# Optimization experiments

Measured on AMD Instinct MI355X. Metric: run time of the kernel, lower is better.

The kernel has to match this reference:

```python
import jax, jax.numpy as jnp
import numpy as np


def setup_inputs() -> dict:
    key = jax.random.key(0)
    k1, k2 = jax.random.split(key)
    B, H, S, D = 2, 16, 2048, 64
    scores = jax.random.normal(k1, (B, H, S, S), dtype=jnp.float32)
    v = jax.random.normal(k2, (B, H, S, D), dtype=jnp.float32)
    return {"scores": scores, "v": v}


def reference(scores, v):
    # softmax over last dim of [B,H,S,S], then contract with V [B,H,S,D]
    prob = jax.nn.softmax(scores, axis=-1)
    return jnp.einsum('bhqk,bhkd->bhqd', prob, v)
```

## Files before the change

kernel.cpp:

```cpp
#include <hip/hip_runtime.h>
#include <hip/hip_bf16.h>

#define NBH     32
#define SEQ     2048
#define DIM     64
#define QBLK    64
#define KBLK    128
#define NCHUNK  (SEQ / KBLK)
#define PSTR    136

typedef __attribute__((ext_vector_type(4))) float f32x4;
typedef __attribute__((ext_vector_type(8))) short bf16x8;

__device__ __forceinline__ unsigned short bfbits(float f) {
    return __builtin_bit_cast(unsigned short, __float2bfloat16(f));
}

__global__ __launch_bounds__(256)
void vprep_kernel(const float* __restrict__ v, unsigned short* __restrict__ wsv)
{
    const int blk = blockIdx.x;
    const int bh  = blk >> 5, tau = blk & 31;
    const float* vp = v + ((size_t)bh * SEQ + tau * 64) * DIM;
    unsigned short* op = wsv + (size_t)blk * 4096;

    for (int fl = threadIdx.x; fl < 512; fl += 256) {
        const int ks1 = fl >> 8, dt = (fl >> 6) & 3, lane = fl & 63;
        const int g = lane >> 4, c = lane & 15;
        const float* sp = vp + (ks1 * 32 + g * 8) * DIM + dt * 16 + c;
        bf16x8 frag;
#pragma unroll
        for (int j = 0; j < 8; ++j)
            frag[j] = (short)bfbits(sp[j * DIM]);
        *reinterpret_cast<bf16x8*>(op + fl * 8) = frag;
    }
}

__global__ __launch_bounds__(256, 2)
void softmaxv_kernel(const float* __restrict__ scores,
                     const unsigned short* __restrict__ vfrags,
                     float* __restrict__ out)
{
    __shared__ unsigned short p_lds[4][2][16 * PSTR];
    __shared__ float l_lds[4][16];

    const int tid  = threadIdx.x;
    const int w    = tid >> 6;
    const int lane = tid & 63;
    const int g    = lane >> 4;
    const int c    = lane & 15;
    const int h    = lane >> 5;
    const int c2   = lane & 31;

    const int bid = blockIdx.x;
    const int nb  = (bid & 7) * (NBH * 32 / 8) + (bid >> 3);
    const int bh  = nb >> 5;
    const int qb  = nb & 31;
    const int q0  = qb * QBLK;

    const float* sp = scores + ((size_t)bh * SEQ + q0 + w * 16 + h) * SEQ + c2 * 4;
    const unsigned short* vb = vfrags + (size_t)bh * 32 * 4096 + lane * 8;

    unsigned short* pb0 = &p_lds[w][0][0];
    unsigned short* pb1 = &p_lds[w][1][0];

    float lsum[8] = {0.f, 0.f, 0.f, 0.f, 0.f, 0.f, 0.f, 0.f};
    f32x4 acc[4];
#pragma unroll
    for (int dt = 0; dt < 4; ++dt) acc[dt] = (f32x4)0.0f;

#define SLOADS(dst, t)                                                         \
    {                                                                          \
        _Pragma("unroll")                                                      \
        for (int j = 0; j < 8; ++j)                                            \
            dst[j] = *reinterpret_cast<const f32x4*>(                          \
                sp + (size_t)(2 * j) * SEQ + (t) * KBLK);                      \
    }

#define VLOAD(vf, t)                                                           \
    {                                                                          \
        _Pragma("unroll")                                                      \
        for (int ks = 0; ks < 4; ++ks)                                         \
            _Pragma("unroll")                                                  \
            for (int dt = 0; dt < 4; ++dt)                                     \
                vf[ks][dt] = *reinterpret_cast<const bf16x8*>(                 \
                    vb + (size_t)(2 * (t) + (ks >> 1)) * 4096 +                \
                    ((ks & 1) * 4 + dt) * 512);                                \
    }

#define PROC(sreg, pbuf)                                                       \
    {                                                                          \
        _Pragma("unroll")                                                      \
        for (int j = 0; j < 8; ++j) {                                          \
            f32x4 s4 = sreg[j];                                                \
            float p0 = __expf(s4[0]);                                          \
            float p1 = __expf(s4[1]);                                          \
            float p2 = __expf(s4[2]);                                          \
            float p3 = __expf(s4[3]);                                          \
            lsum[j] += (p0 + p1) + (p2 + p3);                                  \
            unsigned lo = (unsigned)bfbits(p0) | ((unsigned)bfbits(p1) << 16); \
            unsigned hi = (unsigned)bfbits(p2) | ((unsigned)bfbits(p3) << 16); \
            *reinterpret_cast<uint2*>(&pbuf[(2 * j + h) * PSTR + c2 * 4]) =    \
                make_uint2(lo, hi);                                            \
        }                                                                      \
        _Pragma("unroll")                                                      \
        for (int ks = 0; ks < 4; ++ks) {                                       \
            const bf16x8 a = *reinterpret_cast<const bf16x8*>(                 \
                &pbuf[c * PSTR + ks * 32 + g * 8]);                            \
            _Pragma("unroll")                                                  \
            for (int dt = 0; dt < 4; ++dt)                                     \
                acc[dt] = __builtin_amdgcn_mfma_f32_16x16x32_bf16(             \
                    a, vf[ks][dt], acc[dt], 0, 0, 0);                          \
        }                                                                      \
    }

    f32x4 sA[8], sB[8];
    bf16x8 vf[4][4];
    SLOADS(sA, 0)
    for (int t = 0; t < NCHUNK; t += 2) {
        VLOAD(vf, t)
        SLOADS(sB, t + 1)
        PROC(sA, pb0)
        VLOAD(vf, t + 1)
        if (t + 2 < NCHUNK) SLOADS(sA, t + 2)
        PROC(sB, pb1)
    }
#undef SLOADS
#undef VLOAD
#undef PROC

#pragma unroll
    for (int j = 0; j < 8; ++j) {
        float l = lsum[j];
        l += __shfl_xor(l, 1);
        l += __shfl_xor(l, 2);
        l += __shfl_xor(l, 4);
        l += __shfl_xor(l, 8);
        l += __shfl_xor(l, 16);
        if (c2 == j) l_lds[w][2 * j + h] = l;
    }

    float* op = out + ((size_t)bh * SEQ + q0 + w * 16) * DIM;
    float rl[4];
#pragma unroll
    for (int r = 0; r < 4; ++r)
        rl[r] = 1.0f / l_lds[w][g * 4 + r];
#pragma unroll
    for (int dt = 0; dt < 4; ++dt)
#pragma unroll
        for (int r = 0; r < 4; ++r)
            op[(g * 4 + r) * DIM + dt * 16 + c] = acc[dt][r] * rl[r];
}

extern "C" void kernel_launch(void* const* d_in, const int* in_sizes, int n_in,
                              void* d_out, int out_size, void* d_ws, size_t ws_size,
                              hipStream_t stream)
{
    const float* scores = (const float*)d_in[0];
    const float* v      = (const float*)d_in[1];
    float* out          = (float*)d_out;
    unsigned short* wsv = (unsigned short*)d_ws;

    vprep_kernel<<<dim3(NBH * 32), dim3(256), 0, stream>>>(v, wsv);
    softmaxv_kernel<<<dim3(NBH * (SEQ / QBLK)), dim3(256), 0, stream>>>(scores, wsv, out);
}
```

Before: 137.8 us.

## Compute softmax row sums via MFMA with ones vector and widen key chunks

Each key chunk grows from 128 to 256 columns, so every lane loads full contiguous 16-byte segments across 16 rows. The per-row exp sums are no longer accumulated in scalar registers and reduced with shuffles at the end. An extra MFMA against a vector of bf16 ones accumulates them, and V fragments are streamed in quarter-chunk pieces between MFMA groups. This removes scalar adds and the final cross-lane reduction but adds MFMA work and doubles score register pressure (32 f32x4), which may lower occupancy. The denominator now sums bf16-rounded probabilities rather than fp32 values.

```diff
diff --git a/kernel.cpp b/kernel.cpp
--- a/kernel.cpp
+++ b/kernel.cpp
@@ -5,9 +5,9 @@
 #define SEQ     2048
 #define DIM     64
 #define QBLK    64
-#define KBLK    128
+#define KBLK    256
 #define NCHUNK  (SEQ / KBLK)
-#define PSTR    136
+#define PSTR    264
 
 typedef __attribute__((ext_vector_type(4))) float f32x4;
 typedef __attribute__((ext_vector_type(8))) short bf16x8;
@@ -25,9 +25,9 @@
     unsigned short* op = wsv + (size_t)blk * 4096;
 
     for (int fl = threadIdx.x; fl < 512; fl += 256) {
-        const int ks1 = fl >> 8, dt = (fl >> 6) & 3, lane = fl & 63;
+        const int ks = fl >> 8, dt = (fl >> 6) & 3, lane = fl & 63;
         const int g = lane >> 4, c = lane & 15;
-        const float* sp = vp + (ks1 * 32 + g * 8) * DIM + dt * 16 + c;
+        const float* sp = vp + (ks * 32 + g * 8) * DIM + dt * 16 + c;
         bf16x8 frag;
 #pragma unroll
         for (int j = 0; j < 8; ++j)
@@ -42,109 +42,110 @@
                      float* __restrict__ out)
 {
     __shared__ unsigned short p_lds[4][2][16 * PSTR];
-    __shared__ float l_lds[4][16];
 
     const int tid  = threadIdx.x;
     const int w    = tid >> 6;
     const int lane = tid & 63;
     const int g    = lane >> 4;
     const int c    = lane & 15;
-    const int h    = lane >> 5;
-    const int c2   = lane & 31;
 
     const int bid = blockIdx.x;
-    const int nb  = (bid & 7) * (NBH * 32 / 8) + (bid >> 3);
+    const int nb  = (bid & 7) * 128 + (bid >> 3);
     const int bh  = nb >> 5;
     const int qb  = nb & 31;
     const int q0  = qb * QBLK;
 
-    const float* sp = scores + ((size_t)bh * SEQ + q0 + w * 16 + h) * SEQ + c2 * 4;
+    const float* sp = scores + ((size_t)bh * SEQ + q0 + w * 16) * SEQ + lane * 4;
     const unsigned short* vb = vfrags + (size_t)bh * 32 * 4096 + lane * 8;
 
     unsigned short* pb0 = &p_lds[w][0][0];
     unsigned short* pb1 = &p_lds[w][1][0];
 
-    float lsum[8] = {0.f, 0.f, 0.f, 0.f, 0.f, 0.f, 0.f, 0.f};
     f32x4 acc[4];
 #pragma unroll
     for (int dt = 0; dt < 4; ++dt) acc[dt] = (f32x4)0.0f;
+    f32x4 accl = (f32x4)0.0f;
+    bf16x8 ones;
+#pragma unroll
+    for (int j = 0; j < 8; ++j) ones[j] = (short)0x3F80;
+
+    f32x4 sA[16], sB[16];
+    bf16x8 vf[2][4];
 
 #define SLOADS(dst, t)                                                         \
     {                                                                          \
         _Pragma("unroll")                                                      \
-        for (int j = 0; j < 8; ++j)                                            \
+        for (int j = 0; j < 16; ++j)                                           \
             dst[j] = *reinterpret_cast<const f32x4*>(                          \
-                sp + (size_t)(2 * j) * SEQ + (t) * KBLK);                      \
+                sp + (size_t)j * SEQ + (t) * KBLK);                            \
     }
 
-#define VLOAD(vf, t)                                                           \
+#define VLOAD(tau)                                                             \
     {                                                                          \
         _Pragma("unroll")                                                      \
-        for (int ks = 0; ks < 4; ++ks)                                         \
+        for (int ks = 0; ks < 2; ++ks)                                         \
             _Pragma("unroll")                                                  \
             for (int dt = 0; dt < 4; ++dt)                                     \
                 vf[ks][dt] = *reinterpret_cast<const bf16x8*>(                 \
-                    vb + (size_t)(2 * (t) + (ks >> 1)) * 4096 +                \
-                    ((ks & 1) * 4 + dt) * 512);                                \
+                    vb + (size_t)(tau) * 4096 + (ks * 4 + dt) * 512);          \
     }
 
-#define PROC(sreg, pbuf)                                                       \
+#define HALF(pbuf, half)                                                       \
     {                                                                          \
         _Pragma("unroll")                                                      \
-        for (int j = 0; j < 8; ++j) {                                          \
-            f32x4 s4 = sreg[j];                                                \
+        for (int ks = 0; ks < 2; ++ks) {                                       \
+            const bf16x8 a = *reinterpret_cast<const bf16x8*>(                 \
+                &pbuf[c * PSTR + (half) * 64 + ks * 32 + g * 8]);              \
+            _Pragma("unroll")                                                  \
+            for (int dt = 0; dt < 4; ++dt)                                     \
+                acc[dt] = __builtin_amdgcn_mfma_f32_16x16x32_bf16(             \
+                    a, vf[ks][dt], acc[dt], 0, 0, 0);                          \
+            accl = __builtin_amdgcn_mfma_f32_16x16x32_bf16(                    \
+                a, ones, accl, 0, 0, 0);                                       \
+        }                                                                      \
+    }
+
+#define CHUNK(cur, nxt, t, pbuf, LAST)                                         \
+    {                                                                          \
+        VLOAD(4 * (t))                                                         \
+        if (!(LAST)) SLOADS(nxt, (t) + 1)                                      \
+        _Pragma("unroll")                                                      \
+        for (int j = 0; j < 16; ++j) {                                         \
+            f32x4 s4 = cur[j];                                                 \
             float p0 = __expf(s4[0]);                                          \
             float p1 = __expf(s4[1]);                                          \
             float p2 = __expf(s4[2]);                                          \
             float p3 = __expf(s4[3]);                                          \
-            lsum[j] += (p0 + p1) + (p2 + p3);                                  \
             unsigned lo = (unsigned)bfbits(p0) | ((unsigned)bfbits(p1) << 16); \
             unsigned hi = (unsigned)bfbits(p2) | ((unsigned)bfbits(p3) << 16); \
-            *reinterpret_cast<uint2*>(&pbuf[(2 * j + h) * PSTR + c2 * 4]) =    \
+            *reinterpret_cast<uint2*>(&pbuf[j * PSTR + lane * 4]) =            \
                 make_uint2(lo, hi);                                            \
         }                                                                      \
-        _Pragma("unroll")                                                      \
-        for (int ks = 0; ks < 4; ++ks) {                                       \
-            const bf16x8 a = *reinterpret_cast<const bf16x8*>(                 \
-                &pbuf[c * PSTR + ks * 32 + g * 8]);                            \
-            _Pragma("unroll")                                                  \
-            for (int dt = 0; dt < 4; ++dt)                                     \
-                acc[dt] = __builtin_amdgcn_mfma_f32_16x16x32_bf16(             \
-                    a, vf[ks][dt], acc[dt], 0, 0, 0);                          \
-        }                                                                      \
+        HALF(pbuf, 0)                                                          \
+        VLOAD(4 * (t) + 1)                                                     \
+        HALF(pbuf, 1)                                                          \
+        VLOAD(4 * (t) + 2)                                                     \
+        HALF(pbuf, 2)                                                          \
+        VLOAD(4 * (t) + 3)                                                     \
+        HALF(pbuf, 3)                                                          \
     }
 
-    f32x4 sA[8], sB[8];
-    bf16x8 vf[4][4];
     SLOADS(sA, 0)
     for (int t = 0; t < NCHUNK; t += 2) {
-        VLOAD(vf, t)
-        SLOADS(sB, t + 1)
-        PROC(sA, pb0)
-        VLOAD(vf, t + 1)
-        if (t + 2 < NCHUNK) SLOADS(sA, t + 2)
-        PROC(sB, pb1)
+        CHUNK(sA, sB, t, pb0, 0)
+        CHUNK(sB, sA, t + 1, pb1, (t + 1 == NCHUNK - 1))
     }
 #undef SLOADS
 #undef VLOAD
-#undef PROC
+#undef HALF
+#undef CHUNK
 
-#pragma unroll
-    for (int j = 0; j < 8; ++j) {
-        float l = lsum[j];
-        l += __shfl_xor(l, 1);
-        l += __shfl_xor(l, 2);
-        l += __shfl_xor(l, 4);
-        l += __shfl_xor(l, 8);
-        l += __shfl_xor(l, 16);
-        if (c2 == j) l_lds[w][2 * j + h] = l;
-    }
-
-    float* op = out + ((size_t)bh * SEQ + q0 + w * 16) * DIM;
     float rl[4];
 #pragma unroll
     for (int r = 0; r < 4; ++r)
-        rl[r] = 1.0f / l_lds[w][g * 4 + r];
+        rl[r] = 1.0f / accl[r];
+
+    float* op = out + ((size_t)bh * SEQ + q0 + w * 16) * DIM;
 #pragma unroll
     for (int dt = 0; dt < 4; ++dt)
 #pragma unroll
```

New measurement: 140.1 us. Within noise of the previous version (+1.7%).
